# Kernel optimization log

Hardware: AMD Instinct MI355X
Metric: run time of the kernel (lower is better)

Reference implementation:

```python
import jax, jax.numpy as jnp
import numpy as np

NUM_CLASSES = 10
GAMMA = 1.0
EPS = 1e-12


def setup_inputs() -> dict:
    key = jax.random.key(0)
    k1, k2, k3, k4 = jax.random.split(key, 4)
    x = jax.random.normal(k1, (1024, 64), dtype=jnp.float32)
    exemplars = jax.random.normal(k2, (50000, 64), dtype=jnp.float32)
    exemplar_labels = jax.random.randint(k3, (50000,), 0, NUM_CLASSES)
    # beta_raw initialized as softplus^{-1}(init_beta) with init_beta=1.0
    init_beta = 1.0
    beta_raw = jnp.array([np.log(np.exp(init_beta) - 1.0)], dtype=jnp.float32)
    return {"x": x, "exemplars": exemplars, "exemplar_labels": exemplar_labels,
            "beta_raw": beta_raw}


def reference(x, exemplars, exemplar_labels, beta_raw):
    # Squared Euclidean distances (weight_diag == ones) via GEMM expansion:
    # d2[b, e] = ||x_b||^2 + ||e_e||^2 - 2 <x_b, e_e>
    x2 = jnp.sum(x * x, axis=-1, keepdims=True)            # (B, 1)
    e2 = jnp.sum(exemplars * exemplars, axis=-1)           # (Ne,)
    d2 = x2 + e2[None, :] - 2.0 * (x @ exemplars.T)        # (B, Ne)
    d2 = jnp.maximum(d2, 0.0)  # true sq-dist is nonneg; guards GEMM round-off
    beta = jax.nn.softplus(beta_raw[0])
    sims = jnp.exp(-beta * d2)                              # (B, Ne)
    # scatter-add similarities into per-class bins: (C, B) -> (B, C)
    class_sims = jax.ops.segment_sum(sims.T, exemplar_labels,
                                     num_segments=NUM_CLASSES).T
    logits = GAMMA * jnp.log(class_sims + EPS)
    return logits
```

## Files before the change

kernel.cpp:

```cpp
#include <hip/hip_runtime.h>


#define NB      1024
#define NE      50000
#define NE_PAD  50176
#define NCHUNK  98
#define KD      64
#define NC      10
#define SROWS   64
#define NSTAGE  8
#define LROW    72
#define BCOLS   128

#define LOG2E   1.4426950408889634f

using half8   = __attribute__((ext_vector_type(8))) _Float16;
using half4v  = __attribute__((ext_vector_type(4))) _Float16;
using floatx4 = __attribute__((ext_vector_type(4))) float;

__device__ __forceinline__ float softplus_f(float x) {
  return (x > 20.f) ? x : log1pf(__expf(x));
}

__device__ __forceinline__ float exp2_hw(float x) {
#if __has_builtin(__builtin_amdgcn_exp2f)
  return __builtin_amdgcn_exp2f(x);
#else
  return exp2f(x);
#endif
}

__global__ __launch_bounds__(256) void prep_kernel(
    const float* __restrict__ x, const float* __restrict__ ex,
    const int* __restrict__ labels, const float* __restrict__ beta_raw,
    _Float16* __restrict__ ex_h, float* __restrict__ ce,
    _Float16* __restrict__ x_h, float* __restrict__ cb,
    int* __restrict__ lab_pad)
{
  const int tid = threadIdx.x;
  const float nbeta2 = -softplus_f(beta_raw[0]) * LOG2E;

  const int row = blockIdx.x * 16 + (tid >> 4);
  const int l16 = tid & 15;

  if (row < NE_PAD) {
    float4 v = make_float4(0.f, 0.f, 0.f, 0.f);
    if (row < NE) v = ((const float4*)ex)[row * 16 + l16];
    half4v hv = { (_Float16)v.x, (_Float16)v.y, (_Float16)v.z, (_Float16)v.w };
    *(half4v*)(ex_h + (size_t)row * KD + l16 * 4) = hv;
    float s = v.x*v.x + v.y*v.y + v.z*v.z + v.w*v.w;
    #pragma unroll
    for (int m = 1; m < 16; m <<= 1) s += __shfl_xor(s, m, 64);
    if (l16 == 0) ce[row] = (row < NE) ? (nbeta2 * s) : -1e30f;
    if (l16 == 1) lab_pad[row] = (row < NE) ? labels[row] : 0;
  } else {
    const int rx = row - NE_PAD;
    float4 v = ((const float4*)x)[rx * 16 + l16];
    half4v hv = { (_Float16)v.x, (_Float16)v.y, (_Float16)v.z, (_Float16)v.w };
    *(half4v*)(x_h + (size_t)rx * KD + l16 * 4) = hv;
    float s = v.x*v.x + v.y*v.y + v.z*v.z + v.w*v.w;
    #pragma unroll
    for (int m = 1; m < 16; m <<= 1) s += __shfl_xor(s, m, 64);
    if (l16 == 0) cb[rx] = nbeta2 * s;
  }
}

__global__ __launch_bounds__(256) void main_kernel(
    const _Float16* __restrict__ ex_h, const float* __restrict__ ce,
    const _Float16* __restrict__ x_h, const float* __restrict__ cb,
    const int* __restrict__ lab_pad, const float* __restrict__ beta_raw,
    float* __restrict__ part)
{
  __shared__ _Float16 Ah[2][SROWS * LROW];
  __shared__ float    Ce[2][SROWS];
  __shared__ int      Lb[2][SROWS];

  const int tid  = threadIdx.x;
  const int wave = tid >> 6;
  const int lane = tid & 63;
  const int l15  = lane & 15;
  const int quad = lane >> 4;

  const int btile = blockIdx.x;
  const int chunk = blockIdx.y;
  const int e0    = chunk * 512;
  const int bm0   = btile * BCOLS + wave * 16;
  const int bm1   = bm0 + 64;

  const float beta = softplus_f(beta_raw[0]);
  const float s2 = 2.f * beta * LOG2E;

  const half8* xr0 = (const half8*)(x_h + (size_t)(bm0 + l15) * KD);
  const half8* xr1 = (const half8*)(x_h + (size_t)(bm1 + l15) * KD);
  const half8 bx00 = xr0[quad];
  const half8 bx01 = xr0[quad + 4];
  const half8 bx10 = xr1[quad];
  const half8 bx11 = xr1[quad + 4];
  const float cb0l = cb[bm0 + l15];
  const float cb1l = cb[bm1 + l15];

  const int srow = tid >> 2;
  const int scol = tid & 3;
  const _Float16* gsrc = ex_h + (size_t)(e0 + srow) * KD + scol * 16;
  const int lofs = srow * LROW + scol * 16;

  half8 pr0 = *(const half8*)(gsrc);
  half8 pr1 = *(const half8*)(gsrc + 8);
  float prc = 0.f; int prl = 0;
  if (wave == 0) prc = ce[e0 + lane];
  if (wave == 1) prl = lab_pad[e0 + lane];

  *(half8*)(&Ah[0][lofs])     = pr0;
  *(half8*)(&Ah[0][lofs + 8]) = pr1;
  if (wave == 0) Ce[0][lane] = prc;
  if (wave == 1) Lb[0][lane] = prl;
  __syncthreads();

  floatx4 acc0 = {0.f, 0.f, 0.f, 0.f};
  floatx4 acc1 = {0.f, 0.f, 0.f, 0.f};

  for (int st = 0; st < NSTAGE; ++st) {
    const int b = st & 1;

    if (st + 1 < NSTAGE) {
      const _Float16* g = gsrc + (size_t)(st + 1) * SROWS * KD;
      pr0 = *(const half8*)(g);
      pr1 = *(const half8*)(g + 8);
      if (wave == 0) prc = ce[e0 + (st + 1) * SROWS + lane];
      if (wave == 1) prl = lab_pad[e0 + (st + 1) * SROWS + lane];
    }

    #pragma unroll
    for (int sub = 0; sub < 4; ++sub) {
      const int abase = (sub * 16 + l15) * LROW + quad * 8;
      const half8 ae0 = *(const half8*)(&Ah[b][abase]);
      const half8 ae1 = *(const half8*)(&Ah[b][abase + 32]);
      const float4 ce4 = *(const float4*)(&Ce[b][sub * 16 + quad * 4]);
      const int4   lb4 = *(const int4*)(&Lb[b][sub * 16 + quad * 4]);

      floatx4 d0 = {0.f, 0.f, 0.f, 0.f};
      floatx4 d1 = {0.f, 0.f, 0.f, 0.f};
      d0 = __builtin_amdgcn_mfma_f32_16x16x32_f16(ae0, bx00, d0, 0, 0, 0);
      d0 = __builtin_amdgcn_mfma_f32_16x16x32_f16(ae1, bx01, d0, 0, 0, 0);
      d1 = __builtin_amdgcn_mfma_f32_16x16x32_f16(ae0, bx10, d1, 0, 0, 0);
      d1 = __builtin_amdgcn_mfma_f32_16x16x32_f16(ae1, bx11, d1, 0, 0, 0);

      const float cef[4] = { ce4.x, ce4.y, ce4.z, ce4.w };
      float t0[4], t1[4];
      #pragma unroll
      for (int r = 0; r < 4; ++r) {
        t0[r] = fminf(fmaf(s2, d0[r], cb0l + cef[r]), 0.f);
        t1[r] = fminf(fmaf(s2, d1[r], cb1l + cef[r]), 0.f);
      }

      const float m0 = fmaxf(fmaxf(t0[0], t0[1]), fmaxf(t0[2], t0[3]));
      const float m1 = fmaxf(fmaxf(t1[0], t1[1]), fmaxf(t1[2], t1[3]));
      if (__any(fmaxf(m0, m1) > -25.f)) {
        half4v oh;
        oh[0] = (lb4.x == l15) ? (_Float16)1.f : (_Float16)0.f;
        oh[1] = (lb4.y == l15) ? (_Float16)1.f : (_Float16)0.f;
        oh[2] = (lb4.z == l15) ? (_Float16)1.f : (_Float16)0.f;
        oh[3] = (lb4.w == l15) ? (_Float16)1.f : (_Float16)0.f;

        half4v p0, p1;
        #pragma unroll
        for (int r = 0; r < 4; ++r) {
          p0[r] = (_Float16)exp2_hw(t0[r]);
          p1[r] = (_Float16)exp2_hw(t1[r]);
        }

        acc0 = __builtin_amdgcn_mfma_f32_16x16x16f16(oh, p0, acc0, 0, 0, 0);
        acc1 = __builtin_amdgcn_mfma_f32_16x16x16f16(oh, p1, acc1, 0, 0, 0);
      }
    }

    if (st + 1 < NSTAGE) {
      const int nb = (st + 1) & 1;
      *(half8*)(&Ah[nb][lofs])     = pr0;
      *(half8*)(&Ah[nb][lofs + 8]) = pr1;
      if (wave == 0) Ce[nb][lane] = prc;
      if (wave == 1) Lb[nb][lane] = prl;
      __syncthreads();
    }
  }

  float* dst = part + (size_t)chunk * (NB * NC);
  #pragma unroll
  for (int r = 0; r < 4; ++r) {
    const int c = quad * 4 + r;
    if (c < NC) {
      dst[(bm0 + l15) * NC + c] = acc0[r];
      dst[(bm1 + l15) * NC + c] = acc1[r];
    }
  }
}

__global__ __launch_bounds__(256) void reduce_kernel(
    const float* __restrict__ part, float* __restrict__ out)
{
  const int bc = blockIdx.x * 256 + threadIdx.x;
  if (bc < NB * NC) {
    float s = 0.f;
    #pragma unroll 7
    for (int k = 0; k < NCHUNK; ++k) s += part[(size_t)k * (NB * NC) + bc];
    out[bc] = __logf(s + 1e-12f);
  }
}

extern "C" void kernel_launch(void* const* d_in, const int* in_sizes, int n_in,
                              void* d_out, int out_size, void* d_ws, size_t ws_size,
                              hipStream_t stream)
{
  const float* x        = (const float*)d_in[0];
  const float* ex       = (const float*)d_in[1];
  const int*   labels   = (const int*)d_in[2];
  const float* beta_raw = (const float*)d_in[3];
  float* out = (float*)d_out;

  char* ws = (char*)d_ws;
  _Float16* ex_h    = (_Float16*)ws;
  float*    ce      = (float*)(ws + 6422528);
  _Float16* x_h     = (_Float16*)(ws + 6623232);
  float*    cb      = (float*)(ws + 6754304);
  int*      lab_pad = (int*)(ws + 6758400);
  float*    part    = (float*)(ws + 6959104);

  prep_kernel<<<3200, 256, 0, stream>>>(x, ex, labels, beta_raw,
                                        ex_h, ce, x_h, cb, lab_pad);
  dim3 g(NB / BCOLS, NCHUNK);
  main_kernel<<<g, 256, 0, stream>>>(ex_h, ce, x_h, cb, lab_pad, beta_raw, part);
  reduce_kernel<<<40, 256, 0, stream>>>(part, out);
}
```

Baseline: 94.97 us.

## Fuse fp16 conversion and norm computation into main kernel, drop prep kernel

Removes the separate prep kernel that converted exemplars and x to fp16 and precomputed scaled squared norms and padded labels. The main kernel now loads fp32 exemplars directly, computes their norms with lane shuffles, converts to fp16 while staging into LDS, and handles the tail rows with bounds checks. This saves one launch and a full write-and-reread pass over the fp16 workspace. In exchange each main-kernel block reads twice the bytes per stage and does extra conversion and shuffle work, which runs 8 times redundantly across the batch tiles.

After: 94.47 us. Within noise of the previous version (-0.5%).

```diff
diff --git a/kernel.cpp b/kernel.cpp
--- a/kernel.cpp
+++ b/kernel.cpp
@@ -3,7 +3,6 @@
 
 #define NB      1024
 #define NE      50000
-#define NE_PAD  50176
 #define NCHUNK  98
 #define KD      64
 #define NC      10
@@ -30,45 +29,9 @@
 #endif
 }
 
-__global__ __launch_bounds__(256) void prep_kernel(
+__global__ __launch_bounds__(256) void main_kernel(
     const float* __restrict__ x, const float* __restrict__ ex,
     const int* __restrict__ labels, const float* __restrict__ beta_raw,
-    _Float16* __restrict__ ex_h, float* __restrict__ ce,
-    _Float16* __restrict__ x_h, float* __restrict__ cb,
-    int* __restrict__ lab_pad)
-{
-  const int tid = threadIdx.x;
-  const float nbeta2 = -softplus_f(beta_raw[0]) * LOG2E;
-
-  const int row = blockIdx.x * 16 + (tid >> 4);
-  const int l16 = tid & 15;
-
-  if (row < NE_PAD) {
-    float4 v = make_float4(0.f, 0.f, 0.f, 0.f);
-    if (row < NE) v = ((const float4*)ex)[row * 16 + l16];
-    half4v hv = { (_Float16)v.x, (_Float16)v.y, (_Float16)v.z, (_Float16)v.w };
-    *(half4v*)(ex_h + (size_t)row * KD + l16 * 4) = hv;
-    float s = v.x*v.x + v.y*v.y + v.z*v.z + v.w*v.w;
-    #pragma unroll
-    for (int m = 1; m < 16; m <<= 1) s += __shfl_xor(s, m, 64);
-    if (l16 == 0) ce[row] = (row < NE) ? (nbeta2 * s) : -1e30f;
-    if (l16 == 1) lab_pad[row] = (row < NE) ? labels[row] : 0;
-  } else {
-    const int rx = row - NE_PAD;
-    float4 v = ((const float4*)x)[rx * 16 + l16];
-    half4v hv = { (_Float16)v.x, (_Float16)v.y, (_Float16)v.z, (_Float16)v.w };
-    *(half4v*)(x_h + (size_t)rx * KD + l16 * 4) = hv;
-    float s = v.x*v.x + v.y*v.y + v.z*v.z + v.w*v.w;
-    #pragma unroll
-    for (int m = 1; m < 16; m <<= 1) s += __shfl_xor(s, m, 64);
-    if (l16 == 0) cb[rx] = nbeta2 * s;
-  }
-}
-
-__global__ __launch_bounds__(256) void main_kernel(
-    const _Float16* __restrict__ ex_h, const float* __restrict__ ce,
-    const _Float16* __restrict__ x_h, const float* __restrict__ cb,
-    const int* __restrict__ lab_pad, const float* __restrict__ beta_raw,
     float* __restrict__ part)
 {
   __shared__ _Float16 Ah[2][SROWS * LROW];
@@ -88,32 +51,85 @@
   const int bm1   = bm0 + 64;
 
   const float beta = softplus_f(beta_raw[0]);
-  const float s2 = 2.f * beta * LOG2E;
-
-  const half8* xr0 = (const half8*)(x_h + (size_t)(bm0 + l15) * KD);
-  const half8* xr1 = (const half8*)(x_h + (size_t)(bm1 + l15) * KD);
-  const half8 bx00 = xr0[quad];
-  const half8 bx01 = xr0[quad + 4];
-  const half8 bx10 = xr1[quad];
-  const half8 bx11 = xr1[quad + 4];
-  const float cb0l = cb[bm0 + l15];
-  const float cb1l = cb[bm1 + l15];
+  const float nb2  = -beta * LOG2E;
+  const float s2   = 2.f * beta * LOG2E;
+
+  const float* xr0 = x + (size_t)(bm0 + l15) * KD;
+  const float* xr1 = x + (size_t)(bm1 + l15) * KD;
+  const float4 xa0 = *(const float4*)(xr0 + quad * 8);
+  const float4 xa1 = *(const float4*)(xr0 + quad * 8 + 4);
+  const float4 xa2 = *(const float4*)(xr0 + quad * 8 + 32);
+  const float4 xa3 = *(const float4*)(xr0 + quad * 8 + 36);
+  const float4 xb0 = *(const float4*)(xr1 + quad * 8);
+  const float4 xb1 = *(const float4*)(xr1 + quad * 8 + 4);
+  const float4 xb2 = *(const float4*)(xr1 + quad * 8 + 32);
+  const float4 xb3 = *(const float4*)(xr1 + quad * 8 + 36);
+
+  const half8 bx00 = { (_Float16)xa0.x, (_Float16)xa0.y, (_Float16)xa0.z, (_Float16)xa0.w,
+                       (_Float16)xa1.x, (_Float16)xa1.y, (_Float16)xa1.z, (_Float16)xa1.w };
+  const half8 bx01 = { (_Float16)xa2.x, (_Float16)xa2.y, (_Float16)xa2.z, (_Float16)xa2.w,
+                       (_Float16)xa3.x, (_Float16)xa3.y, (_Float16)xa3.z, (_Float16)xa3.w };
+  const half8 bx10 = { (_Float16)xb0.x, (_Float16)xb0.y, (_Float16)xb0.z, (_Float16)xb0.w,
+                       (_Float16)xb1.x, (_Float16)xb1.y, (_Float16)xb1.z, (_Float16)xb1.w };
+  const half8 bx11 = { (_Float16)xb2.x, (_Float16)xb2.y, (_Float16)xb2.z, (_Float16)xb2.w,
+                       (_Float16)xb3.x, (_Float16)xb3.y, (_Float16)xb3.z, (_Float16)xb3.w };
+
+  float sx0 = xa0.x*xa0.x + xa0.y*xa0.y + xa0.z*xa0.z + xa0.w*xa0.w
+            + xa1.x*xa1.x + xa1.y*xa1.y + xa1.z*xa1.z + xa1.w*xa1.w
+            + xa2.x*xa2.x + xa2.y*xa2.y + xa2.z*xa2.z + xa2.w*xa2.w
+            + xa3.x*xa3.x + xa3.y*xa3.y + xa3.z*xa3.z + xa3.w*xa3.w;
+  float sx1 = xb0.x*xb0.x + xb0.y*xb0.y + xb0.z*xb0.z + xb0.w*xb0.w
+            + xb1.x*xb1.x + xb1.y*xb1.y + xb1.z*xb1.z + xb1.w*xb1.w
+            + xb2.x*xb2.x + xb2.y*xb2.y + xb2.z*xb2.z + xb2.w*xb2.w
+            + xb3.x*xb3.x + xb3.y*xb3.y + xb3.z*xb3.z + xb3.w*xb3.w;
+  sx0 += __shfl_xor(sx0, 16, 64);  sx0 += __shfl_xor(sx0, 32, 64);
+  sx1 += __shfl_xor(sx1, 16, 64);  sx1 += __shfl_xor(sx1, 32, 64);
+  const float cb0l = nb2 * sx0;
+  const float cb1l = nb2 * sx1;
 
   const int srow = tid >> 2;
   const int scol = tid & 3;
-  const _Float16* gsrc = ex_h + (size_t)(e0 + srow) * KD + scol * 16;
   const int lofs = srow * LROW + scol * 16;
 
-  half8 pr0 = *(const half8*)(gsrc);
-  half8 pr1 = *(const half8*)(gsrc + 8);
-  float prc = 0.f; int prl = 0;
-  if (wave == 0) prc = ce[e0 + lane];
-  if (wave == 1) prl = lab_pad[e0 + lane];
-
-  *(half8*)(&Ah[0][lofs])     = pr0;
-  *(half8*)(&Ah[0][lofs + 8]) = pr1;
-  if (wave == 0) Ce[0][lane] = prc;
-  if (wave == 1) Lb[0][lane] = prl;
+  float4 pf0, pf1, pf2, pf3;
+  int    prl;
+  bool   pvalid;
+
+  auto stage_load = [&](int st) {
+    const int grow = e0 + st * SROWS + srow;
+    pvalid = grow < NE;
+    pf0 = make_float4(0.f, 0.f, 0.f, 0.f);
+    pf1 = pf0; pf2 = pf0; pf3 = pf0;
+    prl = 0;
+    if (pvalid) {
+      const float* g = ex + (size_t)grow * KD + scol * 16;
+      pf0 = *(const float4*)(g);
+      pf1 = *(const float4*)(g + 4);
+      pf2 = *(const float4*)(g + 8);
+      pf3 = *(const float4*)(g + 12);
+      if (scol == 1) prl = labels[grow];
+    }
+  };
+
+  auto stage_write = [&](int buf) {
+    float sn = pf0.x*pf0.x + pf0.y*pf0.y + pf0.z*pf0.z + pf0.w*pf0.w
+             + pf1.x*pf1.x + pf1.y*pf1.y + pf1.z*pf1.z + pf1.w*pf1.w
+             + pf2.x*pf2.x + pf2.y*pf2.y + pf2.z*pf2.z + pf2.w*pf2.w
+             + pf3.x*pf3.x + pf3.y*pf3.y + pf3.z*pf3.z + pf3.w*pf3.w;
+    sn += __shfl_xor(sn, 1, 64);
+    sn += __shfl_xor(sn, 2, 64);
+    const half8 h0 = { (_Float16)pf0.x, (_Float16)pf0.y, (_Float16)pf0.z, (_Float16)pf0.w,
+                       (_Float16)pf1.x, (_Float16)pf1.y, (_Float16)pf1.z, (_Float16)pf1.w };
+    const half8 h1 = { (_Float16)pf2.x, (_Float16)pf2.y, (_Float16)pf2.z, (_Float16)pf2.w,
+                       (_Float16)pf3.x, (_Float16)pf3.y, (_Float16)pf3.z, (_Float16)pf3.w };
+    *(half8*)(&Ah[buf][lofs])     = h0;
+    *(half8*)(&Ah[buf][lofs + 8]) = h1;
+    if (scol == 0) Ce[buf][srow] = pvalid ? (nb2 * sn) : -1e30f;
+    if (scol == 1) Lb[buf][srow] = prl;
+  };
+
+  stage_load(0);
+  stage_write(0);
   __syncthreads();
 
   floatx4 acc0 = {0.f, 0.f, 0.f, 0.f};
@@ -122,13 +138,7 @@
   for (int st = 0; st < NSTAGE; ++st) {
     const int b = st & 1;
 
-    if (st + 1 < NSTAGE) {
-      const _Float16* g = gsrc + (size_t)(st + 1) * SROWS * KD;
-      pr0 = *(const half8*)(g);
-      pr1 = *(const half8*)(g + 8);
-      if (wave == 0) prc = ce[e0 + (st + 1) * SROWS + lane];
-      if (wave == 1) prl = lab_pad[e0 + (st + 1) * SROWS + lane];
-    }
+    if (st + 1 < NSTAGE) stage_load(st + 1);
 
     #pragma unroll
     for (int sub = 0; sub < 4; ++sub) {
@@ -175,11 +185,7 @@
     }
 
     if (st + 1 < NSTAGE) {
-      const int nb = (st + 1) & 1;
-      *(half8*)(&Ah[nb][lofs])     = pr0;
-      *(half8*)(&Ah[nb][lofs + 8]) = pr1;
-      if (wave == 0) Ce[nb][lane] = prc;
-      if (wave == 1) Lb[nb][lane] = prl;
+      stage_write((st + 1) & 1);
       __syncthreads();
     }
   }
@@ -217,17 +223,9 @@
   const float* beta_raw = (const float*)d_in[3];
   float* out = (float*)d_out;
 
-  char* ws = (char*)d_ws;
-  _Float16* ex_h    = (_Float16*)ws;
-  float*    ce      = (float*)(ws + 6422528);
-  _Float16* x_h     = (_Float16*)(ws + 6623232);
-  float*    cb      = (float*)(ws + 6754304);
-  int*      lab_pad = (int*)(ws + 6758400);
-  float*    part    = (float*)(ws + 6959104);
-
-  prep_kernel<<<3200, 256, 0, stream>>>(x, ex, labels, beta_raw,
-                                        ex_h, ce, x_h, cb, lab_pad);
+  float* part = (float*)d_ws;
+
   dim3 g(NB / BCOLS, NCHUNK);
-  main_kernel<<<g, 256, 0, stream>>>(ex_h, ce, x_h, cb, lab_pad, beta_raw, part);
+  main_kernel<<<g, 256, 0, stream>>>(x, ex, labels, beta_raw, part);
   reduce_kernel<<<40, 256, 0, stream>>>(part, out);
 }
```
